# Kernel optimization log

Hardware: AMD Instinct MI355X
Metric: run time of the kernel (lower is better)

Reference implementation:

```python
import jax, jax.numpy as jnp
import numpy as np

T, H, F, E, K = 4096, 1024, 2048, 8, 2

def setup_inputs() -> dict:
    key = jax.random.key(0)
    k1, k2, k3, k4, k5, k6 = jax.random.split(key, 6)
    scale = 1.0 / np.sqrt(H)
    return {
        "x": jax.random.normal(k1, (T, H), dtype=jnp.float32),
        "expert_ids": jax.random.randint(k2, (T, K), 0, E, dtype=jnp.int32),
        "expert_weights": jax.random.uniform(k3, (T, K), dtype=jnp.float32),
        "gate_weights": jax.random.normal(k4, (E, H, F), dtype=jnp.float32) * scale,
        "up_weights": jax.random.normal(k5, (E, H, F), dtype=jnp.float32) * scale,
        "down_weights": jax.random.normal(k6, (E, F, H), dtype=jnp.float32) * scale,
    }


def reference(x, expert_ids, expert_weights, gate_weights, up_weights, down_weights):
    # Faithful MoE dispatch/combine. The torch module sorts assignments by
    # expert, runs gate/up/down GEMMs per expert on the gathered tokens, and
    # scatter-adds weight * expert_out back per (token, slot) assignment.
    # Equivalent math: for each expert e, each token accumulates
    # (sum of its routing weights for slots routed to e) * FFN_e(x_token).
    num_experts = gate_weights.shape[0]
    out = jnp.zeros_like(x)
    for e in range(num_experts):
        # coeff[t] = sum_k expert_weights[t,k] * (expert_ids[t,k] == e)
        coeff = jnp.sum(jnp.where(expert_ids == e, expert_weights, 0.0), axis=1)  # [T]
        g = x @ gate_weights[e]           # [T, F]
        u = x @ up_weights[e]             # [T, F]
        y = (jax.nn.silu(g) * u) @ down_weights[e]  # [T, H]
        out = out + coeff[:, None] * y
    return out
```

## Files before the change

kernel.cpp:

```cpp
#include <hip/hip_runtime.h>
#include <hip/hip_bf16.h>

#define Td 4096
#define Hd 1024
#define Fd 2048
#define Ed 8
#define BM 128
#define BN 128
#define BK 64

typedef short bf16x8 __attribute__((ext_vector_type(8)));
typedef float f32x4 __attribute__((ext_vector_type(4)));

__device__ __forceinline__ unsigned short f2bf(float f) {
  union { float f; unsigned u; } v; v.f = f;
  unsigned r = v.u + 0x7FFFu + ((v.u >> 16) & 1u);
  return (unsigned short)(r >> 16);
}

__device__ __forceinline__ void gload16(const unsigned short* g, unsigned short* l) {
  __builtin_amdgcn_global_load_lds(
      (const __attribute__((address_space(1))) unsigned int*)g,
      (__attribute__((address_space(3))) unsigned int*)l,
      16, 0, 0);
}

__global__ void xconv_kernel(const float* __restrict__ x, unsigned short* __restrict__ xb) {
  const int i = (blockIdx.x * 256 + threadIdx.x) * 8;
  const float4 v0 = *(const float4*)(x + i);
  const float4 v1 = *(const float4*)(x + i + 4);
  bf16x8 o;
  o[0] = (short)f2bf(v0.x); o[1] = (short)f2bf(v0.y);
  o[2] = (short)f2bf(v0.z); o[3] = (short)f2bf(v0.w);
  o[4] = (short)f2bf(v1.x); o[5] = (short)f2bf(v1.y);
  o[6] = (short)f2bf(v1.z); o[7] = (short)f2bf(v1.w);
  *(bf16x8*)(xb + i) = o;
}

__global__ void prep_transpose_kernel(const float* __restrict__ gw,
                                      const float* __restrict__ uw,
                                      const float* __restrict__ dw,
                                      unsigned short* __restrict__ gt,
                                      unsigned short* __restrict__ ut,
                                      unsigned short* __restrict__ dt) {
  const int m = blockIdx.z % 3;
  const int e = blockIdx.z / 3;
  const int R = (m == 2) ? Fd : Hd;
  const int C = (m == 2) ? Hd : Fd;
  const int r0 = blockIdx.y * 64, c0 = blockIdx.x * 64;
  if (r0 >= R || c0 >= C) return;
  const float* src = ((m == 0) ? gw : (m == 1) ? uw : dw) + (size_t)e * Hd * Fd;
  unsigned short* dst = ((m == 0) ? gt : (m == 1) ? ut : dt) + (size_t)e * Hd * Fd;
  __shared__ unsigned short tile[64][68];
  const int tr = threadIdx.x >> 4;
  const int tc = (threadIdx.x & 15) * 4;
#pragma unroll
  for (int i = 0; i < 4; ++i) {
    const int r = tr + i * 16;
    const float4 v = *(const float4*)(src + (size_t)(r0 + r) * C + c0 + tc);
    tile[r][tc + 0] = f2bf(v.x);
    tile[r][tc + 1] = f2bf(v.y);
    tile[r][tc + 2] = f2bf(v.z);
    tile[r][tc + 3] = f2bf(v.w);
  }
  __syncthreads();
#pragma unroll
  for (int i = 0; i < 4; ++i) {
    const int c = tr + i * 16;
    ushort4 o;
    o.x = tile[tc + 0][c];
    o.y = tile[tc + 1][c];
    o.z = tile[tc + 2][c];
    o.w = tile[tc + 3][c];
    *(ushort4*)(dst + (size_t)(c0 + c) * R + r0 + tc) = o;
  }
}

__global__ void routing_kernel(const int* __restrict__ ids,
                               const float* __restrict__ w,
                               int* __restrict__ cnt, int* __restrict__ base,
                               int* __restrict__ tok, float* __restrict__ cof) {
  __shared__ int lcnt[Ed], lbase[Ed], lpos[Ed];
  const int t = threadIdx.x;
  const int lane = t & 63;
  if (t < Ed) { lcnt[t] = 0; lpos[t] = 0; }
  __syncthreads();
  for (int i = t; i < Td; i += 1024) {
    const int e0 = ids[2 * i], e1 = ids[2 * i + 1];
    const int em = (e1 == e0) ? -1 : e1;
#pragma unroll
    for (int e = 0; e < Ed; ++e) {
      unsigned long long m0 = __ballot(e0 == e);
      unsigned long long m1 = __ballot(em == e);
      int n = __popcll(m0) + __popcll(m1);
      if (lane == 0 && n) atomicAdd(&lcnt[e], n);
    }
  }
  __syncthreads();
  if (t == 0) {
    int s = 0;
    for (int e = 0; e < Ed; ++e) { lbase[e] = s; s += lcnt[e]; }
  }
  __syncthreads();
  const unsigned long long below = (1ull << lane) - 1ull;
  for (int i = t; i < Td; i += 1024) {
    const int e0 = ids[2 * i], e1 = ids[2 * i + 1];
    const float w0 = w[2 * i], w1 = w[2 * i + 1];
    const bool mg = (e1 == e0);
    const int em = mg ? -1 : e1;
#pragma unroll
    for (int e = 0; e < Ed; ++e) {
      unsigned long long m0 = __ballot(e0 == e);
      unsigned long long m1 = __ballot(em == e);
      const int n0 = __popcll(m0);
      const int n = n0 + __popcll(m1);
      int p = 0;
      if (lane == 0 && n) p = atomicAdd(&lpos[e], n);
      p = __shfl(p, 0);
      if (e0 == e) {
        const int r = lbase[e] + p + __popcll(m0 & below);
        tok[r] = i; cof[r] = mg ? (w0 + w1) : w0;
      }
      if (em == e) {
        const int r = lbase[e] + p + n0 + __popcll(m1 & below);
        tok[r] = i; cof[r] = w1;
      }
    }
  }
  __syncthreads();
  if (t < Ed) { cnt[t] = lcnt[t]; base[t] = lbase[t]; }
}

__global__ __launch_bounds__(256)
void gateup_kernel(const unsigned short* __restrict__ xb,
                   const unsigned short* __restrict__ gate_t,
                   const int* __restrict__ cnt, const int* __restrict__ base,
                   const int* __restrict__ tok, const float* __restrict__ cof,
                   unsigned short* __restrict__ act) {
  const int e = blockIdx.z, mt = blockIdx.y, nt = blockIdx.x;
  const int cn = cnt[e];
  if (mt * BM >= cn) return;
  const int b0 = base[e];

  __shared__ unsigned short A_lds[BM * BK];
  __shared__ unsigned short Bg_lds[BN * BK];
  __shared__ unsigned short Bu_lds[BN * BK];
  __shared__ int tok_l[BM];
  __shared__ float cof_l[BM];

  const int tid = threadIdx.x;
  if (tid < BM) {
    const int r = mt * BM + tid;
    tok_l[tid] = (r < cn) ? tok[b0 + r] : 0;
    cof_l[tid] = (r < cn) ? cof[b0 + r] : 0.f;
  }
  __syncthreads();

  const int lane = tid & 63;
  const int wave = tid >> 6;
  const int wm = wave >> 1, wn = wave & 1;
  const int fr16 = lane & 15;
  const int jb = lane >> 4;
  const int rx7 = lane & 7;

  const int sw = ((lane & 7) ^ (lane >> 3)) * 8;
  const unsigned short* gwp = gate_t + (size_t)e * Fd * Hd;
  const unsigned short* ap[4];
  const unsigned short* gp[4];
#pragma unroll
  for (int i = 0; i < 4; ++i) {
    const int rl = wave * 32 + i * 8 + (lane >> 3);
    ap[i] = xb + (size_t)tok_l[rl] * Hd + sw;
    gp[i] = gwp + (size_t)(nt * BN + rl) * Hd + sw;
  }
  const size_t UPOFF = (size_t)Ed * Fd * Hd;

  f32x4 accg[4][4], accu[4][4];
#pragma unroll
  for (int i = 0; i < 4; ++i)
#pragma unroll
    for (int j = 0; j < 4; ++j) {
      accg[i][j] = (f32x4){0.f, 0.f, 0.f, 0.f};
      accu[i][j] = (f32x4){0.f, 0.f, 0.f, 0.f};
    }

  for (int k0 = 0; k0 < Hd; k0 += BK) {
    __syncthreads();
#pragma unroll
    for (int i = 0; i < 4; ++i) {
      gload16(ap[i] + k0,         A_lds  + wave * 2048 + i * 512);
      gload16(gp[i] + k0,         Bg_lds + wave * 2048 + i * 512);
      gload16(gp[i] + UPOFF + k0, Bu_lds + wave * 2048 + i * 512);
    }
    __syncthreads();
#pragma unroll
    for (int kk = 0; kk < 2; ++kk) {
      bf16x8 af[4], bg[4], bu[4];
      const int slot = kk * 4 + jb;
#pragma unroll
      for (int f = 0; f < 4; ++f) {
        const int ra = wm * 64 + f * 16 + fr16;
        const int rb = wn * 64 + f * 16 + fr16;
        af[f] = *(const bf16x8*)&A_lds [64 * ra + 8 * (slot ^ rx7)];
        bg[f] = *(const bf16x8*)&Bg_lds[64 * rb + 8 * (slot ^ rx7)];
        bu[f] = *(const bf16x8*)&Bu_lds[64 * rb + 8 * (slot ^ rx7)];
      }
#pragma unroll
      for (int fm = 0; fm < 4; ++fm)
#pragma unroll
        for (int fn = 0; fn < 4; ++fn) {
          accg[fm][fn] = __builtin_amdgcn_mfma_f32_16x16x32_bf16(af[fm], bg[fn], accg[fm][fn], 0, 0, 0);
          accu[fm][fn] = __builtin_amdgcn_mfma_f32_16x16x32_bf16(af[fm], bu[fn], accu[fm][fn], 0, 0, 0);
        }
    }
  }

  const int row4 = (lane >> 4) * 4;
#pragma unroll
  for (int fm = 0; fm < 4; ++fm) {
#pragma unroll
    for (int fn = 0; fn < 4; ++fn) {
#pragma unroll
      for (int r = 0; r < 4; ++r) {
        const int rr = wm * 64 + fm * 16 + row4 + r;
        const int grow = mt * BM + rr;
        if (grow < cn) {
          const float g = accg[fm][fn][r];
          const float u = accu[fm][fn][r];
          const float a = (g / (1.f + __expf(-g))) * u * cof_l[rr];
          const int col = nt * BN + wn * 64 + fn * 16 + fr16;
          act[(size_t)(b0 + grow) * Fd + col] = f2bf(a);
        }
      }
    }
  }
}

__global__ __launch_bounds__(256)
void down_kernel(const unsigned short* __restrict__ act,
                 const unsigned short* __restrict__ down_t,
                 const int* __restrict__ cnt, const int* __restrict__ base,
                 const int* __restrict__ tok,
                 float* __restrict__ out) {
  const int e = blockIdx.z, mt = blockIdx.y, nt = blockIdx.x;
  const int cn = cnt[e];
  if (mt * BM >= cn) return;
  const int b0 = base[e];

  __shared__ unsigned short A_lds[BM * BK];
  __shared__ unsigned short B_lds[BN * BK];
  __shared__ int tok_l[BM];

  const int tid = threadIdx.x;
  if (tid < BM) {
    const int r = mt * BM + tid;
    tok_l[tid] = (r < cn) ? tok[b0 + r] : 0;
  }

  const int lane = tid & 63;
  const int wave = tid >> 6;
  const int wm = wave >> 1, wn = wave & 1;
  const int fr16 = lane & 15;
  const int jb = lane >> 4;
  const int rx7 = lane & 7;

  const int sw = ((lane & 7) ^ (lane >> 3)) * 8;
  const unsigned short* dwp = down_t + (size_t)e * Hd * Fd;
  const unsigned short* ap[4];
  const unsigned short* bp[4];
#pragma unroll
  for (int i = 0; i < 4; ++i) {
    const int rl = wave * 32 + i * 8 + (lane >> 3);
    int rowg = b0 + mt * BM + rl;
    if (rowg > 8191) rowg = 8191;
    ap[i] = act + (size_t)rowg * Fd + sw;
    bp[i] = dwp + (size_t)(nt * BN + rl) * Fd + sw;
  }

  f32x4 acc[4][4];
#pragma unroll
  for (int i = 0; i < 4; ++i)
#pragma unroll
    for (int j = 0; j < 4; ++j) acc[i][j] = (f32x4){0.f, 0.f, 0.f, 0.f};

  for (int k0 = 0; k0 < Fd; k0 += BK) {
    __syncthreads();
#pragma unroll
    for (int i = 0; i < 4; ++i) {
      gload16(ap[i] + k0, A_lds + wave * 2048 + i * 512);
      gload16(bp[i] + k0, B_lds + wave * 2048 + i * 512);
    }
    __syncthreads();
#pragma unroll
    for (int kk = 0; kk < 2; ++kk) {
      bf16x8 af[4], bf[4];
      const int slot = kk * 4 + jb;
#pragma unroll
      for (int f = 0; f < 4; ++f) {
        const int ra = wm * 64 + f * 16 + fr16;
        const int rb = wn * 64 + f * 16 + fr16;
        af[f] = *(const bf16x8*)&A_lds[64 * ra + 8 * (slot ^ rx7)];
        bf[f] = *(const bf16x8*)&B_lds[64 * rb + 8 * (slot ^ rx7)];
      }
#pragma unroll
      for (int fm = 0; fm < 4; ++fm)
#pragma unroll
        for (int fn = 0; fn < 4; ++fn)
          acc[fm][fn] = __builtin_amdgcn_mfma_f32_16x16x32_bf16(af[fm], bf[fn], acc[fm][fn], 0, 0, 0);
    }
  }

  const int row4 = (lane >> 4) * 4;
#pragma unroll
  for (int fm = 0; fm < 4; ++fm) {
#pragma unroll
    for (int fn = 0; fn < 4; ++fn) {
#pragma unroll
      for (int r = 0; r < 4; ++r) {
        const int rr = wm * 64 + fm * 16 + row4 + r;
        if (mt * BM + rr < cn) {
          const int col = nt * BN + wn * 64 + fn * 16 + fr16;
          atomicAdd(&out[(size_t)tok_l[rr] * Hd + col], acc[fm][fn][r]);
        }
      }
    }
  }
}

extern "C" void kernel_launch(void* const* d_in, const int* in_sizes, int n_in,
                              void* d_out, int out_size, void* d_ws, size_t ws_size,
                              hipStream_t stream) {
  const float* x  = (const float*)d_in[0];
  const int*   ids = (const int*)d_in[1];
  const float* w  = (const float*)d_in[2];
  const float* gw = (const float*)d_in[3];
  const float* uw = (const float*)d_in[4];
  const float* dw = (const float*)d_in[5];
  float* out = (float*)d_out;

  const size_t SZW = (size_t)Ed * Hd * Fd * 2;
  const size_t ACT = (size_t)8192 * Fd * 2;
  const size_t XB  = (size_t)Td * Hd * 2;
  const size_t NEED = 3 * SZW + ACT + XB + 1 * 1024 * 1024;
  if (ws_size < NEED) return;

  char* ws = (char*)d_ws;
  unsigned short* gt   = (unsigned short*)(ws);
  unsigned short* ut   = (unsigned short*)(ws + SZW);
  unsigned short* dt   = (unsigned short*)(ws + 2 * SZW);
  unsigned short* act  = (unsigned short*)(ws + 3 * SZW);
  unsigned short* xbuf = (unsigned short*)(ws + 3 * SZW + ACT);
  char* meta = ws + 3 * SZW + ACT + XB;
  int*   cnt  = (int*)meta;
  int*   base = (int*)(meta + 32);
  int*   tok  = (int*)(meta + 64);
  float* cof  = (float*)(meta + 64 + 8192 * 4);

  hipMemsetAsync(d_out, 0, (size_t)Td * Hd * 4, stream);
  xconv_kernel<<<Td * Hd / 8 / 256, 256, 0, stream>>>(x, xbuf);
  routing_kernel<<<1, 1024, 0, stream>>>(ids, w, cnt, base, tok, cof);
  prep_transpose_kernel<<<dim3(32, 32, 24), 256, 0, stream>>>(gw, uw, dw, gt, ut, dt);
  gateup_kernel<<<dim3(Fd / BN, Td / BM, Ed), 256, 0, stream>>>(xbuf, gt, cnt, base, tok, cof, act);
  down_kernel<<<dim3(Hd / BN, Td / BM, Ed), 256, 0, stream>>>(act, dt, cnt, base, tok, out);
}
```

Measured before the change: 439.6 us.

## Interleave gate/up weights and add triple-buffered 256x128 GEMM pipeline with split-K down

Gate and up weight rows are interleaved into one transposed buffer so a single B tile feeds both GEMMs, and the SiLU*up pairing is done with a lane shuffle in the epilogue. Both expert GEMMs move to 256x128x32 tiles with a three-stage global-to-LDS pipeline, explicit waitcnt/barrier scheduling and MFMA priority boosts, and the down GEMM is split into two K halves accumulated via atomics. The aim is to hide memory latency and improve MFMA utilisation and occupancy, at the cost of more atomic traffic and fragile hand-tuned synchronisation. The grid y-dimension is sized to cover each expert's token count.

```diff
diff --git a/kernel.cpp b/kernel.cpp
--- a/kernel.cpp
+++ b/kernel.cpp
@@ -5,9 +5,10 @@
 #define Hd 1024
 #define Fd 2048
 #define Ed 8
-#define BM 128
-#define BN 128
-#define BK 64
+
+#define BMq 256
+#define BNq 128
+#define BKq 32
 
 typedef short bf16x8 __attribute__((ext_vector_type(8)));
 typedef float f32x4 __attribute__((ext_vector_type(4)));
@@ -40,8 +41,7 @@
 __global__ void prep_transpose_kernel(const float* __restrict__ gw,
                                       const float* __restrict__ uw,
                                       const float* __restrict__ dw,
-                                      unsigned short* __restrict__ gt,
-                                      unsigned short* __restrict__ ut,
+                                      unsigned short* __restrict__ gu,
                                       unsigned short* __restrict__ dt) {
   const int m = blockIdx.z % 3;
   const int e = blockIdx.z / 3;
@@ -50,7 +50,6 @@
   const int r0 = blockIdx.y * 64, c0 = blockIdx.x * 64;
   if (r0 >= R || c0 >= C) return;
   const float* src = ((m == 0) ? gw : (m == 1) ? uw : dw) + (size_t)e * Hd * Fd;
-  unsigned short* dst = ((m == 0) ? gt : (m == 1) ? ut : dt) + (size_t)e * Hd * Fd;
   __shared__ unsigned short tile[64][68];
   const int tr = threadIdx.x >> 4;
   const int tc = (threadIdx.x & 15) * 4;
@@ -72,7 +71,10 @@
     o.y = tile[tc + 1][c];
     o.z = tile[tc + 2][c];
     o.w = tile[tc + 3][c];
-    *(ushort4*)(dst + (size_t)(c0 + c) * R + r0 + tc) = o;
+    size_t drow = (m == 2) ? (size_t)(c0 + c) : (size_t)(2 * (c0 + c) + m);
+    unsigned short* dst = (m == 2) ? (dt + (size_t)e * Hd * Fd)
+                                   : (gu + (size_t)e * 2 * Fd * Hd);
+    *(ushort4*)(dst + drow * R + r0 + tc) = o;
   }
 }
 
@@ -131,196 +133,292 @@
   if (t < Ed) { cnt[t] = lcnt[t]; base[t] = lbase[t]; }
 }
 
-__global__ __launch_bounds__(256)
+
+__global__ __launch_bounds__(256, 2)
 void gateup_kernel(const unsigned short* __restrict__ xb,
-                   const unsigned short* __restrict__ gate_t,
+                   const unsigned short* __restrict__ gu_t,
                    const int* __restrict__ cnt, const int* __restrict__ base,
                    const int* __restrict__ tok, const float* __restrict__ cof,
                    unsigned short* __restrict__ act) {
   const int e = blockIdx.z, mt = blockIdx.y, nt = blockIdx.x;
   const int cn = cnt[e];
-  if (mt * BM >= cn) return;
+  if (mt * BMq >= cn) return;
   const int b0 = base[e];
 
-  __shared__ unsigned short A_lds[BM * BK];
-  __shared__ unsigned short Bg_lds[BN * BK];
-  __shared__ unsigned short Bu_lds[BN * BK];
-  __shared__ int tok_l[BM];
-  __shared__ float cof_l[BM];
-
-  const int tid = threadIdx.x;
-  if (tid < BM) {
-    const int r = mt * BM + tid;
-    tok_l[tid] = (r < cn) ? tok[b0 + r] : 0;
+  __shared__ unsigned short A_l[3][BMq * BKq];
+  __shared__ unsigned short B_l[3][BNq * BKq];
+  __shared__ int tok_l[BMq];
+  __shared__ float cof_l[BMq];
+
+  const int tid = threadIdx.x, lane = tid & 63, wave = tid >> 6;
+  {
+    const int r = mt * BMq + tid;
+    tok_l[tid] = (r < cn) ? tok[b0 + r] : tok[b0];
     cof_l[tid] = (r < cn) ? cof[b0 + r] : 0.f;
   }
   __syncthreads();
 
-  const int lane = tid & 63;
-  const int wave = tid >> 6;
+  const unsigned short* gup = gu_t + (size_t)e * 2 * Fd * Hd + (size_t)(nt * BNq) * Hd;
+  const unsigned short* aS[4];
+  const unsigned short* bS[2];
+#pragma unroll
+  for (int j = 0; j < 4; ++j) {
+    const int s = tid + j * 256;
+    const int row = s >> 2, g = (s & 3) ^ ((row >> 1) & 3);
+    aS[j] = xb + (size_t)tok_l[row] * Hd + g * 8;
+  }
+#pragma unroll
+  for (int j = 0; j < 2; ++j) {
+    const int s = tid + j * 256;
+    const int row = s >> 2, g = (s & 3) ^ ((row >> 1) & 3);
+    bS[j] = gup + (size_t)row * Hd + g * 8;
+  }
+  const int dstA = wave * 512;
+  const int dstB = wave * 512;
+
+  const int fr16 = lane & 15, kg = lane >> 4;
   const int wm = wave >> 1, wn = wave & 1;
-  const int fr16 = lane & 15;
-  const int jb = lane >> 4;
-  const int rx7 = lane & 7;
-
-  const int sw = ((lane & 7) ^ (lane >> 3)) * 8;
-  const unsigned short* gwp = gate_t + (size_t)e * Fd * Hd;
-  const unsigned short* ap[4];
-  const unsigned short* gp[4];
-#pragma unroll
-  for (int i = 0; i < 4; ++i) {
-    const int rl = wave * 32 + i * 8 + (lane >> 3);
-    ap[i] = xb + (size_t)tok_l[rl] * Hd + sw;
-    gp[i] = gwp + (size_t)(nt * BN + rl) * Hd + sw;
-  }
-  const size_t UPOFF = (size_t)Ed * Fd * Hd;
-
-  f32x4 accg[4][4], accu[4][4];
-#pragma unroll
-  for (int i = 0; i < 4; ++i)
-#pragma unroll
-    for (int j = 0; j < 4; ++j) {
-      accg[i][j] = (f32x4){0.f, 0.f, 0.f, 0.f};
-      accu[i][j] = (f32x4){0.f, 0.f, 0.f, 0.f};
-    }
-
-  for (int k0 = 0; k0 < Hd; k0 += BK) {
-    __syncthreads();
-#pragma unroll
-    for (int i = 0; i < 4; ++i) {
-      gload16(ap[i] + k0,         A_lds  + wave * 2048 + i * 512);
-      gload16(gp[i] + k0,         Bg_lds + wave * 2048 + i * 512);
-      gload16(gp[i] + UPOFF + k0, Bu_lds + wave * 2048 + i * 512);
-    }
-    __syncthreads();
-#pragma unroll
-    for (int kk = 0; kk < 2; ++kk) {
-      bf16x8 af[4], bg[4], bu[4];
-      const int slot = kk * 4 + jb;
-#pragma unroll
-      for (int f = 0; f < 4; ++f) {
-        const int ra = wm * 64 + f * 16 + fr16;
-        const int rb = wn * 64 + f * 16 + fr16;
-        af[f] = *(const bf16x8*)&A_lds [64 * ra + 8 * (slot ^ rx7)];
-        bg[f] = *(const bf16x8*)&Bg_lds[64 * rb + 8 * (slot ^ rx7)];
-        bu[f] = *(const bf16x8*)&Bu_lds[64 * rb + 8 * (slot ^ rx7)];
-      }
-#pragma unroll
-      for (int fm = 0; fm < 4; ++fm)
-#pragma unroll
-        for (int fn = 0; fn < 4; ++fn) {
-          accg[fm][fn] = __builtin_amdgcn_mfma_f32_16x16x32_bf16(af[fm], bg[fn], accg[fm][fn], 0, 0, 0);
-          accu[fm][fn] = __builtin_amdgcn_mfma_f32_16x16x32_bf16(af[fm], bu[fn], accu[fm][fn], 0, 0, 0);
-        }
-    }
+  int aOff[8], bOff[4];
+#pragma unroll
+  for (int rf = 0; rf < 8; ++rf) {
+    const int r = wm * 128 + rf * 16 + fr16;
+    aOff[rf] = r * 32 + ((kg ^ ((r >> 1) & 3)) * 8);
+  }
+#pragma unroll
+  for (int cf = 0; cf < 4; ++cf) {
+    const int r = wn * 64 + cf * 16 + fr16;
+    bOff[cf] = r * 32 + ((kg ^ ((r >> 1) & 3)) * 8);
+  }
+
+  f32x4 acc[8][4];
+#pragma unroll
+  for (int i = 0; i < 8; ++i)
+#pragma unroll
+    for (int j = 0; j < 4; ++j) acc[i][j] = (f32x4){0.f, 0.f, 0.f, 0.f};
+
+  const int NT = Hd / BKq;
+#pragma unroll
+  for (int j = 0; j < 4; ++j) gload16(aS[j] + 0, &A_l[0][j * 2048 + dstA]);
+#pragma unroll
+  for (int j = 0; j < 2; ++j) gload16(bS[j] + 0, &B_l[0][j * 2048 + dstB]);
+#pragma unroll
+  for (int j = 0; j < 4; ++j) gload16(aS[j] + BKq, &A_l[1][j * 2048 + dstA]);
+#pragma unroll
+  for (int j = 0; j < 2; ++j) gload16(bS[j] + BKq, &B_l[1][j * 2048 + dstB]);
+  asm volatile("s_waitcnt vmcnt(6)" ::: "memory");
+  __builtin_amdgcn_s_barrier();
+
+  for (int t = 0; t < NT; ++t) {
+    const int sl = t % 3, sn = (t + 2) % 3;
+    const bool st = (t + 2) < NT;
+    const int kn = (t + 2) * BKq;
+    const unsigned short* Ab = &A_l[sl][0];
+    const unsigned short* Bb = &B_l[sl][0];
+    bf16x8 av[4], bv[4];
+#pragma unroll
+    for (int rf = 0; rf < 4; ++rf) av[rf] = *(const bf16x8*)(Ab + aOff[rf]);
+#pragma unroll
+    for (int cf = 0; cf < 4; ++cf) bv[cf] = *(const bf16x8*)(Bb + bOff[cf]);
+    if (st) {
+      gload16(aS[0] + kn, &A_l[sn][0 * 2048 + dstA]);
+      gload16(aS[1] + kn, &A_l[sn][1 * 2048 + dstA]);
+      gload16(bS[0] + kn, &B_l[sn][0 * 2048 + dstB]);
+    }
+    __builtin_amdgcn_s_barrier();
+    asm volatile("s_waitcnt lgkmcnt(0)" ::: "memory");
+    __builtin_amdgcn_sched_barrier(0);
+    __builtin_amdgcn_s_setprio(1);
+#pragma unroll
+    for (int rf = 0; rf < 4; ++rf)
+#pragma unroll
+      for (int cf = 0; cf < 4; ++cf)
+        acc[rf][cf] = __builtin_amdgcn_mfma_f32_16x16x32_bf16(av[rf], bv[cf], acc[rf][cf], 0, 0, 0);
+    __builtin_amdgcn_s_setprio(0);
+    __builtin_amdgcn_s_barrier();
+    bf16x8 aw[4];
+#pragma unroll
+    for (int rf = 0; rf < 4; ++rf) aw[rf] = *(const bf16x8*)(Ab + aOff[4 + rf]);
+    if (st) {
+      gload16(aS[2] + kn, &A_l[sn][2 * 2048 + dstA]);
+      gload16(aS[3] + kn, &A_l[sn][3 * 2048 + dstA]);
+      gload16(bS[1] + kn, &B_l[sn][1 * 2048 + dstB]);
+    }
+    __builtin_amdgcn_s_barrier();
+    asm volatile("s_waitcnt lgkmcnt(0)" ::: "memory");
+    __builtin_amdgcn_sched_barrier(0);
+    __builtin_amdgcn_s_setprio(1);
+#pragma unroll
+    for (int rf = 0; rf < 4; ++rf)
+#pragma unroll
+      for (int cf = 0; cf < 4; ++cf)
+        acc[4 + rf][cf] = __builtin_amdgcn_mfma_f32_16x16x32_bf16(aw[rf], bv[cf], acc[4 + rf][cf], 0, 0, 0);
+    __builtin_amdgcn_s_setprio(0);
+    if (t < NT - 2)       asm volatile("s_waitcnt vmcnt(6)" ::: "memory");
+    else if (t == NT - 2) asm volatile("s_waitcnt vmcnt(0)" ::: "memory");
+    __builtin_amdgcn_s_barrier();
   }
 
   const int row4 = (lane >> 4) * 4;
-#pragma unroll
-  for (int fm = 0; fm < 4; ++fm) {
-#pragma unroll
-    for (int fn = 0; fn < 4; ++fn) {
+  const int colbase = nt * BNq + wn * 64;
+#pragma unroll
+  for (int rf = 0; rf < 8; ++rf) {
+#pragma unroll
+    for (int cf = 0; cf < 4; ++cf) {
 #pragma unroll
       for (int r = 0; r < 4; ++r) {
-        const int rr = wm * 64 + fm * 16 + row4 + r;
-        const int grow = mt * BM + rr;
-        if (grow < cn) {
-          const float g = accg[fm][fn][r];
-          const float u = accu[fm][fn][r];
+        const int rr = wm * 128 + rf * 16 + row4 + r;
+        const int grow = mt * BMq + rr;
+        const float v = acc[rf][cf][r];
+        const float p = __shfl_xor(v, 1);
+        const float g = (lane & 1) ? p : v;
+        const float u = (lane & 1) ? v : p;
+        if (grow < cn && !(lane & 1)) {
           const float a = (g / (1.f + __expf(-g))) * u * cof_l[rr];
-          const int col = nt * BN + wn * 64 + fn * 16 + fr16;
-          act[(size_t)(b0 + grow) * Fd + col] = f2bf(a);
+          const int col = colbase + cf * 16 + fr16;
+          act[(size_t)(b0 + grow) * Fd + (col >> 1)] = f2bf(a);
         }
       }
     }
   }
 }
 
-__global__ __launch_bounds__(256)
+__global__ __launch_bounds__(256, 2)
 void down_kernel(const unsigned short* __restrict__ act,
                  const unsigned short* __restrict__ down_t,
                  const int* __restrict__ cnt, const int* __restrict__ base,
                  const int* __restrict__ tok,
                  float* __restrict__ out) {
-  const int e = blockIdx.z, mt = blockIdx.y, nt = blockIdx.x;
+  const int nt = blockIdx.x & 7, kc = blockIdx.x >> 3;
+  const int e = blockIdx.z, mt = blockIdx.y;
   const int cn = cnt[e];
-  if (mt * BM >= cn) return;
+  if (mt * BMq >= cn) return;
   const int b0 = base[e];
 
-  __shared__ unsigned short A_lds[BM * BK];
-  __shared__ unsigned short B_lds[BN * BK];
-  __shared__ int tok_l[BM];
-
-  const int tid = threadIdx.x;
-  if (tid < BM) {
-    const int r = mt * BM + tid;
-    tok_l[tid] = (r < cn) ? tok[b0 + r] : 0;
-  }
-
-  const int lane = tid & 63;
-  const int wave = tid >> 6;
+  __shared__ unsigned short A_l[3][BMq * BKq];
+  __shared__ unsigned short B_l[3][BNq * BKq];
+  __shared__ int tok_l[BMq];
+
+  const int tid = threadIdx.x, lane = tid & 63, wave = tid >> 6;
+  {
+    const int r = mt * BMq + tid;
+    tok_l[tid] = (r < cn) ? tok[b0 + r] : tok[b0];
+  }
+  __syncthreads();
+
+  const int kbase = kc * (Fd / 2);
+  const unsigned short* dwp = down_t + (size_t)e * Hd * Fd + (size_t)(nt * BNq) * Fd + kbase;
+  const unsigned short* aS[4];
+  const unsigned short* bS[2];
+#pragma unroll
+  for (int j = 0; j < 4; ++j) {
+    const int s = tid + j * 256;
+    const int row = s >> 2, g = (s & 3) ^ ((row >> 1) & 3);
+    int ar = b0 + mt * BMq + row;
+    if (ar > 8191) ar = 8191;
+    aS[j] = act + (size_t)ar * Fd + kbase + g * 8;
+  }
+#pragma unroll
+  for (int j = 0; j < 2; ++j) {
+    const int s = tid + j * 256;
+    const int row = s >> 2, g = (s & 3) ^ ((row >> 1) & 3);
+    bS[j] = dwp + (size_t)row * Fd + g * 8;
+  }
+  const int dstA = wave * 512, dstB = wave * 512;
+
+  const int fr16 = lane & 15, kg = lane >> 4;
   const int wm = wave >> 1, wn = wave & 1;
-  const int fr16 = lane & 15;
-  const int jb = lane >> 4;
-  const int rx7 = lane & 7;
-
-  const int sw = ((lane & 7) ^ (lane >> 3)) * 8;
-  const unsigned short* dwp = down_t + (size_t)e * Hd * Fd;
-  const unsigned short* ap[4];
-  const unsigned short* bp[4];
-#pragma unroll
-  for (int i = 0; i < 4; ++i) {
-    const int rl = wave * 32 + i * 8 + (lane >> 3);
-    int rowg = b0 + mt * BM + rl;
-    if (rowg > 8191) rowg = 8191;
-    ap[i] = act + (size_t)rowg * Fd + sw;
-    bp[i] = dwp + (size_t)(nt * BN + rl) * Fd + sw;
-  }
-
-  f32x4 acc[4][4];
-#pragma unroll
-  for (int i = 0; i < 4; ++i)
+  int aOff[8], bOff[4];
+#pragma unroll
+  for (int rf = 0; rf < 8; ++rf) {
+    const int r = wm * 128 + rf * 16 + fr16;
+    aOff[rf] = r * 32 + ((kg ^ ((r >> 1) & 3)) * 8);
+  }
+#pragma unroll
+  for (int cf = 0; cf < 4; ++cf) {
+    const int r = wn * 64 + cf * 16 + fr16;
+    bOff[cf] = r * 32 + ((kg ^ ((r >> 1) & 3)) * 8);
+  }
+
+  f32x4 acc[8][4];
+#pragma unroll
+  for (int i = 0; i < 8; ++i)
 #pragma unroll
     for (int j = 0; j < 4; ++j) acc[i][j] = (f32x4){0.f, 0.f, 0.f, 0.f};
 
-  for (int k0 = 0; k0 < Fd; k0 += BK) {
-    __syncthreads();
-#pragma unroll
-    for (int i = 0; i < 4; ++i) {
-      gload16(ap[i] + k0, A_lds + wave * 2048 + i * 512);
-      gload16(bp[i] + k0, B_lds + wave * 2048 + i * 512);
-    }
-    __syncthreads();
-#pragma unroll
-    for (int kk = 0; kk < 2; ++kk) {
-      bf16x8 af[4], bf[4];
-      const int slot = kk * 4 + jb;
-#pragma unroll
-      for (int f = 0; f < 4; ++f) {
-        const int ra = wm * 64 + f * 16 + fr16;
-        const int rb = wn * 64 + f * 16 + fr16;
-        af[f] = *(const bf16x8*)&A_lds[64 * ra + 8 * (slot ^ rx7)];
-        bf[f] = *(const bf16x8*)&B_lds[64 * rb + 8 * (slot ^ rx7)];
-      }
-#pragma unroll
-      for (int fm = 0; fm < 4; ++fm)
-#pragma unroll
-        for (int fn = 0; fn < 4; ++fn)
-          acc[fm][fn] = __builtin_amdgcn_mfma_f32_16x16x32_bf16(af[fm], bf[fn], acc[fm][fn], 0, 0, 0);
-    }
+  const int NT = (Fd / 2) / BKq;
+#pragma unroll
+  for (int j = 0; j < 4; ++j) gload16(aS[j] + 0, &A_l[0][j * 2048 + dstA]);
+#pragma unroll
+  for (int j = 0; j < 2; ++j) gload16(bS[j] + 0, &B_l[0][j * 2048 + dstB]);
+#pragma unroll
+  for (int j = 0; j < 4; ++j) gload16(aS[j] + BKq, &A_l[1][j * 2048 + dstA]);
+#pragma unroll
+  for (int j = 0; j < 2; ++j) gload16(bS[j] + BKq, &B_l[1][j * 2048 + dstB]);
+  asm volatile("s_waitcnt vmcnt(6)" ::: "memory");
+  __builtin_amdgcn_s_barrier();
+
+  for (int t = 0; t < NT; ++t) {
+    const int sl = t % 3, sn = (t + 2) % 3;
+    const bool st = (t + 2) < NT;
+    const int kn = (t + 2) * BKq;
+    const unsigned short* Ab = &A_l[sl][0];
+    const unsigned short* Bb = &B_l[sl][0];
+    bf16x8 av[4], bv[4];
+#pragma unroll
+    for (int rf = 0; rf < 4; ++rf) av[rf] = *(const bf16x8*)(Ab + aOff[rf]);
+#pragma unroll
+    for (int cf = 0; cf < 4; ++cf) bv[cf] = *(const bf16x8*)(Bb + bOff[cf]);
+    if (st) {
+      gload16(aS[0] + kn, &A_l[sn][0 * 2048 + dstA]);
+      gload16(aS[1] + kn, &A_l[sn][1 * 2048 + dstA]);
+      gload16(bS[0] + kn, &B_l[sn][0 * 2048 + dstB]);
+    }
+    __builtin_amdgcn_s_barrier();
+    asm volatile("s_waitcnt lgkmcnt(0)" ::: "memory");
+    __builtin_amdgcn_sched_barrier(0);
+    __builtin_amdgcn_s_setprio(1);
+#pragma unroll
+    for (int rf = 0; rf < 4; ++rf)
+#pragma unroll
+      for (int cf = 0; cf < 4; ++cf)
+        acc[rf][cf] = __builtin_amdgcn_mfma_f32_16x16x32_bf16(av[rf], bv[cf], acc[rf][cf], 0, 0, 0);
+    __builtin_amdgcn_s_setprio(0);
+    __builtin_amdgcn_s_barrier();
+    bf16x8 aw[4];
+#pragma unroll
+    for (int rf = 0; rf < 4; ++rf) aw[rf] = *(const bf16x8*)(Ab + aOff[4 + rf]);
+    if (st) {
+      gload16(aS[2] + kn, &A_l[sn][2 * 2048 + dstA]);
+      gload16(aS[3] + kn, &A_l[sn][3 * 2048 + dstA]);
+      gload16(bS[1] + kn, &B_l[sn][1 * 2048 + dstB]);
+    }
+    __builtin_amdgcn_s_barrier();
+    asm volatile("s_waitcnt lgkmcnt(0)" ::: "memory");
+    __builtin_amdgcn_sched_barrier(0);
+    __builtin_amdgcn_s_setprio(1);
+#pragma unroll
+    for (int rf = 0; rf < 4; ++rf)
+#pragma unroll
+      for (int cf = 0; cf < 4; ++cf)
+        acc[4 + rf][cf] = __builtin_amdgcn_mfma_f32_16x16x32_bf16(aw[rf], bv[cf], acc[4 + rf][cf], 0, 0, 0);
+    __builtin_amdgcn_s_setprio(0);
+    if (t < NT - 2)       asm volatile("s_waitcnt vmcnt(6)" ::: "memory");
+    else if (t == NT - 2) asm volatile("s_waitcnt vmcnt(0)" ::: "memory");
+    __builtin_amdgcn_s_barrier();
   }
 
   const int row4 = (lane >> 4) * 4;
-#pragma unroll
-  for (int fm = 0; fm < 4; ++fm) {
-#pragma unroll
-    for (int fn = 0; fn < 4; ++fn) {
+  const int colbase = nt * BNq + wn * 64;
+#pragma unroll
+  for (int rf = 0; rf < 8; ++rf) {
+#pragma unroll
+    for (int cf = 0; cf < 4; ++cf) {
 #pragma unroll
       for (int r = 0; r < 4; ++r) {
-        const int rr = wm * 64 + fm * 16 + row4 + r;
-        if (mt * BM + rr < cn) {
-          const int col = nt * BN + wn * 64 + fn * 16 + fr16;
-          atomicAdd(&out[(size_t)tok_l[rr] * Hd + col], acc[fm][fn][r]);
+        const int rr = wm * 128 + rf * 16 + row4 + r;
+        if (mt * BMq + rr < cn) {
+          const int col = colbase + cf * 16 + fr16;
+          atomicAdd(&out[(size_t)tok_l[rr] * Hd + col], acc[rf][cf][r]);
         }
       }
     }
@@ -345,8 +443,7 @@
   if (ws_size < NEED) return;
 
   char* ws = (char*)d_ws;
-  unsigned short* gt   = (unsigned short*)(ws);
-  unsigned short* ut   = (unsigned short*)(ws + SZW);
+  unsigned short* gu   = (unsigned short*)(ws);
   unsigned short* dt   = (unsigned short*)(ws + 2 * SZW);
   unsigned short* act  = (unsigned short*)(ws + 3 * SZW);
   unsigned short* xbuf = (unsigned short*)(ws + 3 * SZW + ACT);
@@ -359,7 +456,7 @@
   hipMemsetAsync(d_out, 0, (size_t)Td * Hd * 4, stream);
   xconv_kernel<<<Td * Hd / 8 / 256, 256, 0, stream>>>(x, xbuf);
   routing_kernel<<<1, 1024, 0, stream>>>(ids, w, cnt, base, tok, cof);
-  prep_transpose_kernel<<<dim3(32, 32, 24), 256, 0, stream>>>(gw, uw, dw, gt, ut, dt);
-  gateup_kernel<<<dim3(Fd / BN, Td / BM, Ed), 256, 0, stream>>>(xbuf, gt, cnt, base, tok, cof, act);
-  down_kernel<<<dim3(Hd / BN, Td / BM, Ed), 256, 0, stream>>>(act, dt, cnt, base, tok, out);
-}
+  prep_transpose_kernel<<<dim3(32, 32, 24), 256, 0, stream>>>(gw, uw, dw, gu, dt);
+  gateup_kernel<<<dim3(2 * Fd / BNq, Td * 2 / BMq, Ed), 256, 0, stream>>>(xbuf, gu, cnt, base, tok, cof, act);
+  down_kernel<<<dim3((Hd / BNq) * 2, Td * 2 / BMq, Ed), 256, 0, stream>>>(act, dt, cnt, base, tok, out);
+}
```

Measured after the change: 428.6 us. 2.5% less time.
